# Optimization experiments

Hardware: AMD Instinct MI355X
Metric: run time of the kernel (lower is better)

## Reference

```python
import jax, jax.numpy as jnp
import numpy as np

B, T, H, L, O = 256, 512, 512, 2, 2

def setup_inputs() -> dict:
    key = jax.random.key(0)
    ks = jax.random.split(key, 9)
    s = 0.05
    return {
        "x": jax.random.normal(ks[0], (B, T), jnp.float32),
        # input-side gate weights, layer 0 (input dim 1); gate order: [r, z, n]
        "Wi0": jax.random.normal(ks[1], (3, H, 1), jnp.float32) * s,
        "bi0": jax.random.normal(ks[2], (3, H), jnp.float32) * s,
        # input-side gate weights, layers 1..L-1 (input dim H)
        "Wi_rest": jax.random.normal(ks[3], (L - 1, 3, H, H), jnp.float32) * s,
        "bi_rest": jax.random.normal(ks[4], (L - 1, 3, H), jnp.float32) * s,
        # hidden-side gate weights for all layers
        "Wh": jax.random.normal(ks[5], (L, 3, H, H), jnp.float32) * s,
        "bh": jax.random.normal(ks[6], (L, 3, H), jnp.float32) * s,
        "fc_w": jax.random.normal(ks[7], (O, H), jnp.float32) * s,
        "fc_b": jax.random.normal(ks[8], (O,), jnp.float32) * s,
    }


def reference(x, Wi0, bi0, Wi_rest, bi_rest, Wh, bh, fc_w, fc_b):
    nL = Wh.shape[0]
    hsz = Wh.shape[-1]
    bsz = x.shape[0]

    def step(h, x_t):  # h: [L, B, H], x_t: [B]
        inp = x_t[:, None]  # [B, 1]
        new_h = []
        for l in range(nL):
            # fuse the 3 input-side and 3 hidden-side gate GEMMs into one einsum each
            if l == 0:
                gi = jnp.einsum('bi,ghi->gbh', inp, Wi0) + bi0[:, None, :]
            else:
                gi = jnp.einsum('bi,ghi->gbh', inp, Wi_rest[l - 1]) + bi_rest[l - 1, :, None, :]
            gh = jnp.einsum('bi,ghi->gbh', h[l], Wh[l]) + bh[l, :, None, :]
            r = jax.nn.sigmoid(gi[0] + gh[0])
            z = jax.nn.sigmoid(gi[1] + gh[1])
            n = jnp.tanh(gi[2] + r * gh[2])
            hl = (1.0 - z) * n + z * h[l]
            new_h.append(hl)
            inp = hl
        return jnp.stack(new_h), None

    h0 = jnp.zeros((nL, bsz, hsz), x.dtype)
    h_final, _ = jax.lax.scan(step, h0, x.T)  # scan over time axis
    return h_final[-1] @ fc_w.T + fc_b  # [B, O]
```

## Files before the change

### kernel.cpp

```cpp
#include <hip/hip_runtime.h>


#define TLEN 512
#define HDIM 512
#define MROW 32
#define NL0  8
#define WPG  24
#define GRID 192
#define U0   64
#define U1   32
#define HSZ  (MROW*HDIM)
#define ROWB 1040
#define DEPTH 4

#define RT_BAR 10000000ULL

typedef __attribute__((ext_vector_type(8))) short bf16x8;
typedef __attribute__((ext_vector_type(4))) float f32x4;

#define AT_LD64(p)   __hip_atomic_load((const unsigned long long*)(p), __ATOMIC_RELAXED, __HIP_MEMORY_SCOPE_AGENT)
#define AT_LD32(p)   __hip_atomic_load((const unsigned*)(p), __ATOMIC_RELAXED, __HIP_MEMORY_SCOPE_AGENT)
#define AT_ST16(p,v) __hip_atomic_store((unsigned short*)(p), (v), __ATOMIC_RELAXED, __HIP_MEMORY_SCOPE_AGENT)
#define AT_ST32(p,v) __hip_atomic_store((unsigned*)(p), (v), __ATOMIC_RELAXED, __HIP_MEMORY_SCOPE_AGENT)
#define AT_ST32F(p,v) __hip_atomic_store((float*)(p), (v), __ATOMIC_RELAXED, __HIP_MEMORY_SCOPE_AGENT)

__device__ __forceinline__ unsigned short f2bf(float f){
  unsigned u = __builtin_bit_cast(unsigned, f);
  u = (u + 0x7FFFu + ((u>>16)&1u)) >> 16;
  return (unsigned short)u;
}
__device__ __forceinline__ float sigm(float v){ return __builtin_amdgcn_rcpf(1.f + __expf(-v)); }
__device__ __forceinline__ float tanh_f(float v){ return 1.f - 2.f*__builtin_amdgcn_rcpf(__expf(2.f*v)+1.f); }

__device__ __forceinline__ bool wait_flags(unsigned* fl, int tA, int tB, int* sab){
  if (threadIdx.x < 64){
    const int lane = threadIdx.x;
    const int tgt = (lane<8) ? tA : (lane<24 ? tB : (int)0x80000000);
    const unsigned long long t0 = __builtin_amdgcn_s_memrealtime();
    int ab = 0;
    for(;;){
      int f = (lane<24) ? (int)AT_LD32(fl + lane*16) : 0x7fffffff;
      if (__ballot(f >= tgt) == ~0ULL) break;
      if (__builtin_amdgcn_s_memrealtime() - t0 > RT_BAR){ ab = 1; break; }
      __builtin_amdgcn_s_sleep(1);
    }
    if (lane==0) *sab = ab;
  }
  __syncthreads();
  __builtin_amdgcn_sched_barrier(0);
  return *sab != 0;
}

__device__ __forceinline__ void stage16(const unsigned short* src, unsigned short* shDst, int tid){
  unsigned long long hb[16];
  #pragma unroll
  for (int i=0;i<16;++i)
    hb[i] = AT_LD64((const char*)src + tid*8 + i*2048);
  #pragma unroll
  for (int i=0;i<16;++i){
    int flat = tid*8 + i*2048;
    *(unsigned long long*)((char*)shDst + (flat>>10)*ROWB + (flat&1023)) = hb[i];
  }
}

extern "C" __global__ void __launch_bounds__(256,1)
gru_persistent(const float* __restrict__ x,
               const float* __restrict__ Wi0,
               const float* __restrict__ bi0,
               const float* __restrict__ Wi1,
               const float* __restrict__ bi1,
               const float* __restrict__ Wh,
               const float* __restrict__ bh,
               const float* __restrict__ fcw,
               const float* __restrict__ fcb,
               float* __restrict__ out,
               unsigned* __restrict__ flg,
               unsigned short* __restrict__ h0g,
               unsigned short* __restrict__ h1g,
               float* __restrict__ h1f)
{
  __shared__ unsigned short shA[MROW*(ROWB/2)];
  __shared__ unsigned short shB[MROW*(ROWB/2)];
  __shared__ float shG[MROW*192];
  __shared__ int s_ab;

  const int tid  = threadIdx.x;
  const int lane = tid & 63;
  const int w    = tid >> 6;
  const int grp  = blockIdx.x & 7;
  const int wgid = blockIdx.x >> 3;
  const int g32  = grp*32;

  unsigned* fl = flg + grp*512;
  unsigned short* h0 = h0g + grp*DEPTH*HSZ;
  unsigned short* h1 = h1g + grp*DEPTH*HSZ;

  if (wgid < NL0){
    const int u0   = wgid*U0;
    const int colb = w*48;

    bf16x8 bfr[3][16];
    #pragma unroll
    for (int nt=0; nt<3; ++nt){
      int col = colb + nt*16 + (lane&15);
      int g = col>>6, uu = col&63;
      const float* wrow = Wh + (size_t)(g*HDIM + u0 + uu)*HDIM;
      #pragma unroll
      for (int ks=0; ks<16; ++ks){
        int k = ks*32 + (lane>>4)*8;
        const float4 f0 = *(const float4*)(wrow + k);
        const float4 f1 = *(const float4*)(wrow + k + 4);
        bf16x8 v;
        v[0]=(short)f2bf(f0.x); v[1]=(short)f2bf(f0.y); v[2]=(short)f2bf(f0.z); v[3]=(short)f2bf(f0.w);
        v[4]=(short)f2bf(f1.x); v[5]=(short)f2bf(f1.y); v[6]=(short)f2bf(f1.z); v[7]=(short)f2bf(f1.w);
        bfr[nt][ks]=v;
      }
    }
    const int ua   = tid & 63;
    const int brow = (tid>>6)*8;
    float wi0v[3], bi0v[3], bh0v[3];
    #pragma unroll
    for (int g=0; g<3; ++g){
      wi0v[g] = Wi0[g*HDIM + u0+ua];
      bi0v[g] = bi0[g*HDIM + u0+ua];
      bh0v[g] = bh [g*HDIM + u0+ua];
    }
    float h_own[8];
    #pragma unroll
    for (int j=0;j<8;++j) h_own[j]=0.f;

    for (int s=0; s<TLEN; ++s){
      float xv[8];
      #pragma unroll
      for (int j=0;j<8;++j) xv[j] = x[(g32+brow+j)*TLEN + s];

      if (wait_flags(fl, s, s-3, &s_ab)) return;

      stage16(h0 + ((s-1)&3)*HSZ, shA, tid);
      __syncthreads();
      f32x4 acc[2][3] = {};
      #pragma unroll
      for (int ks=0; ks<16; ++ks){
        int koff = ks*64 + (lane>>4)*16;
        bf16x8 a0 = *(const bf16x8*)((const char*)shA + (lane&15)*ROWB + koff);
        bf16x8 a1 = *(const bf16x8*)((const char*)shA + ((lane&15)+16)*ROWB + koff);
        #pragma unroll
        for (int nt=0; nt<3; ++nt){
          acc[0][nt] = __builtin_amdgcn_mfma_f32_16x16x32_bf16(a0, bfr[nt][ks], acc[0][nt],0,0,0);
          acc[1][nt] = __builtin_amdgcn_mfma_f32_16x16x32_bf16(a1, bfr[nt][ks], acc[1][nt],0,0,0);
        }
      }
      #pragma unroll
      for (int mt=0; mt<2; ++mt)
        #pragma unroll
        for (int nt=0; nt<3; ++nt)
          #pragma unroll
          for (int j=0;j<4;++j){
            int b = mt*16 + (lane>>4)*4 + j;
            shG[b*192 + colb + nt*16 + (lane&15)] = acc[mt][nt][j];
          }
      __syncthreads();
      unsigned short* dstA = h0 + (s&3)*HSZ;
      #pragma unroll
      for (int j=0;j<8;++j){
        int b = brow + j;
        float G0 = shG[b*192 + ua]       + bh0v[0];
        float G1 = shG[b*192 + 64 + ua]  + bh0v[1];
        float G2 = shG[b*192 + 128 + ua] + bh0v[2];
        float r_ = sigm(fmaf(xv[j], wi0v[0], bi0v[0]) + G0);
        float z_ = sigm(fmaf(xv[j], wi0v[1], bi0v[1]) + G1);
        float n_ = tanh_f(fmaf(xv[j], wi0v[2], bi0v[2]) + r_*G2);
        float hn = (1.f - z_)*n_ + z_*h_own[j];
        h_own[j] = hn;
        AT_ST16(&dstA[b*HDIM + u0 + ua], f2bf(hn));
      }
      asm volatile("s_waitcnt vmcnt(0)" ::: "memory");
      __syncthreads();
      if (tid==0) AT_ST32(fl + wgid*16, (unsigned)(s+1));
    }
    if (wgid==0){
      if (wait_flags(fl, (int)0x80000000, TLEN, &s_ab)) return;
      int p = tid>>2, kl = tid&3;
      int b = p>>1, o = p&1;
      const char* h8 = (const char*)(h1f + (size_t)(g32+b)*HDIM + kl*128);
      const float2* w2 = (const float2*)(fcw + o*HDIM + kl*128);
      float a2 = 0.f;
      #pragma unroll
      for (int k=0;k<64;++k){
        unsigned long long v = AT_LD64(h8 + k*8);
        float2 hv = __builtin_bit_cast(float2, v);
        float2 wv = w2[k];
        a2 = fmaf(hv.x, wv.x, fmaf(hv.y, wv.y, a2));
      }
      a2 += __shfl_xor(a2, 1);
      a2 += __shfl_xor(a2, 2);
      if (kl==0) out[(g32+b)*2 + o] = a2 + fcb[o];
    }
  } else {
    const int u1   = (wgid-NL0)*U1;
    const int colb = (w<2) ? w*48 : 96 + (w-2)*48;

    bf16x8 bfr[3][16];
    #pragma unroll
    for (int nt=0; nt<3; ++nt){
      int col = colb + nt*16 + (lane&15);
      const float* wrow;
      if (w < 2){ int g = col>>5, uu = col&31;
        wrow = Wi1 + (size_t)(g*HDIM + u1 + uu)*HDIM;
      } else {    int c2 = col-96; int g = c2>>5, uu = c2&31;
        wrow = Wh + (size_t)((3+g)*HDIM + u1 + uu)*HDIM;
      }
      #pragma unroll
      for (int ks=0; ks<16; ++ks){
        int k = ks*32 + (lane>>4)*8;
        const float4 f0 = *(const float4*)(wrow + k);
        const float4 f1 = *(const float4*)(wrow + k + 4);
        bf16x8 v;
        v[0]=(short)f2bf(f0.x); v[1]=(short)f2bf(f0.y); v[2]=(short)f2bf(f0.z); v[3]=(short)f2bf(f0.w);
        v[4]=(short)f2bf(f1.x); v[5]=(short)f2bf(f1.y); v[6]=(short)f2bf(f1.z); v[7]=(short)f2bf(f1.w);
        bfr[nt][ks]=v;
      }
    }
    const int ua   = tid & 31;
    const int brow = (tid>>5)*4;
    float bi1v[3], bh1v[3];
    #pragma unroll
    for (int g=0; g<3; ++g){
      bi1v[g] = bi1[g*HDIM + u1+ua];
      bh1v[g] = bh [(3+g)*HDIM + u1+ua];
    }
    float h_own[4];
    #pragma unroll
    for (int j=0;j<4;++j) h_own[j]=0.f;

    for (int t=1; t<=TLEN; ++t){
      const unsigned short* srcA = h0 + ((t-1)&3)*HSZ;
      const unsigned short* srcB = h1 + ((t-2)&3)*HSZ;

      if (wait_flags(fl, (int)0x80000000, t-1, &s_ab)) return;
      unsigned long long hb1[16];
      #pragma unroll
      for (int i=0;i<16;++i)
        hb1[i] = AT_LD64((const char*)srcB + tid*8 + i*2048);

      if (wait_flags(fl, t, (int)0x80000000, &s_ab)) return;
      unsigned long long hb0[16];
      #pragma unroll
      for (int i=0;i<16;++i)
        hb0[i] = AT_LD64((const char*)srcA + tid*8 + i*2048);

      #pragma unroll
      for (int i=0;i<16;++i){
        int flat = tid*8 + i*2048;
        *(unsigned long long*)((char*)shA + (flat>>10)*ROWB + (flat&1023)) = hb0[i];
        *(unsigned long long*)((char*)shB + (flat>>10)*ROWB + (flat&1023)) = hb1[i];
      }
      __syncthreads();
      const char* shSrc = (w<2) ? (const char*)shA : (const char*)shB;
      f32x4 acc[2][3] = {};
      #pragma unroll
      for (int ks=0; ks<16; ++ks){
        int koff = ks*64 + (lane>>4)*16;
        bf16x8 a0 = *(const bf16x8*)(shSrc + (lane&15)*ROWB + koff);
        bf16x8 a1 = *(const bf16x8*)(shSrc + ((lane&15)+16)*ROWB + koff);
        #pragma unroll
        for (int nt=0; nt<3; ++nt){
          acc[0][nt] = __builtin_amdgcn_mfma_f32_16x16x32_bf16(a0, bfr[nt][ks], acc[0][nt],0,0,0);
          acc[1][nt] = __builtin_amdgcn_mfma_f32_16x16x32_bf16(a1, bfr[nt][ks], acc[1][nt],0,0,0);
        }
      }
      #pragma unroll
      for (int mt=0; mt<2; ++mt)
        #pragma unroll
        for (int nt=0; nt<3; ++nt)
          #pragma unroll
          for (int j=0;j<4;++j){
            int b = mt*16 + (lane>>4)*4 + j;
            shG[b*192 + colb + nt*16 + (lane&15)] = acc[mt][nt][j];
          }
      __syncthreads();
      unsigned short* dstB = h1 + ((t-1)&3)*HSZ;
      #pragma unroll
      for (int j=0;j<4;++j){
        int b = brow + j;
        float gi0 = shG[b*192 + ua]        + bi1v[0];
        float gi1 = shG[b*192 + 32 + ua]   + bi1v[1];
        float gi2 = shG[b*192 + 64 + ua]   + bi1v[2];
        float gh0 = shG[b*192 + 96 + ua]   + bh1v[0];
        float gh1 = shG[b*192 + 128 + ua]  + bh1v[1];
        float gh2 = shG[b*192 + 160 + ua]  + bh1v[2];
        float r_ = sigm(gi0+gh0);
        float z_ = sigm(gi1+gh1);
        float n_ = tanh_f(gi2 + r_*gh2);
        float hn = (1.f - z_)*n_ + z_*h_own[j];
        h_own[j] = hn;
        AT_ST16(&dstB[b*HDIM + u1 + ua], f2bf(hn));
        if (t == TLEN) AT_ST32F(&h1f[(size_t)(g32+b)*HDIM + u1 + ua], hn);
      }
      asm volatile("s_waitcnt vmcnt(0)" ::: "memory");
      __syncthreads();
      if (tid==0) AT_ST32(fl + wgid*16, (unsigned)t);
    }
  }
}

extern "C" void kernel_launch(void* const* d_in, const int* in_sizes, int n_in,
                              void* d_out, int out_size, void* d_ws, size_t ws_size,
                              hipStream_t stream)
{
  const float* x   = (const float*)d_in[0];
  const float* Wi0 = (const float*)d_in[1];
  const float* bi0 = (const float*)d_in[2];
  const float* Wi1 = (const float*)d_in[3];
  const float* bi1 = (const float*)d_in[4];
  const float* Wh  = (const float*)d_in[5];
  const float* bh  = (const float*)d_in[6];
  const float* fcw = (const float*)d_in[7];
  const float* fcb = (const float*)d_in[8];
  float* out = (float*)d_out;

  unsigned*       flg = (unsigned*)d_ws;
  unsigned short* h0g = (unsigned short*)((char*)d_ws + 16384);
  unsigned short* h1g = (unsigned short*)((char*)d_ws + 16384 + 1048576);
  float*          h1f = (float*)((char*)d_ws + 16384 + 2*1048576);

  hipMemsetAsync(d_ws, 0, 16384 + 2*1048576 + 524288, stream);
  gru_persistent<<<GRID, 256, 0, stream>>>(x,Wi0,bi0,Wi1,bi1,Wh,bh,fcw,fcb,out,
                                           flg,h0g,h1g,h1f);
}
```

Before: 2.420 ms.

## Split batch into 16 groups of 16 rows, doubling persistent workgroups

Halves the batch rows per group from 32 to 16 and doubles the number of independent groups, so the grid grows to 384 workgroups at two per CU. Each workgroup does half the MFMA work and half the staging loads per timestep, which shortens the serial per-step critical path. Odd groups start after a short delay to stagger their flag polling. The cost is duplicated weight registers across twice as many workgroups, two workgroups sharing each CU, and more flag-polling traffic.

```diff
diff --git a/kernel.cpp b/kernel.cpp
--- a/kernel.cpp
+++ b/kernel.cpp
@@ -3,13 +3,13 @@
 
 #define TLEN 512
 #define HDIM 512
-#define MROW 32
+#define MROW 16
 #define NL0  8
-#define WPG  24
-#define GRID 192
+#define NGRP 16
+#define GRID 384
 #define U0   64
 #define U1   32
-#define HSZ  (MROW*HDIM)
+#define HSZE (MROW*HDIM)
 #define ROWB 1040
 #define DEPTH 4
 
@@ -51,19 +51,19 @@
   return *sab != 0;
 }
 
-__device__ __forceinline__ void stage16(const unsigned short* src, unsigned short* shDst, int tid){
-  unsigned long long hb[16];
+__device__ __forceinline__ void stage8(const unsigned short* src, unsigned short* shDst, int tid){
+  unsigned long long hb[8];
   #pragma unroll
-  for (int i=0;i<16;++i)
+  for (int i=0;i<8;++i)
     hb[i] = AT_LD64((const char*)src + tid*8 + i*2048);
   #pragma unroll
-  for (int i=0;i<16;++i){
+  for (int i=0;i<8;++i){
     int flat = tid*8 + i*2048;
     *(unsigned long long*)((char*)shDst + (flat>>10)*ROWB + (flat&1023)) = hb[i];
   }
 }
 
-extern "C" __global__ void __launch_bounds__(256,1)
+extern "C" __global__ void __launch_bounds__(256,2)
 gru_persistent(const float* __restrict__ x,
                const float* __restrict__ Wi0,
                const float* __restrict__ bi0,
@@ -87,13 +87,19 @@
   const int tid  = threadIdx.x;
   const int lane = tid & 63;
   const int w    = tid >> 6;
-  const int grp  = blockIdx.x & 7;
-  const int wgid = blockIdx.x >> 3;
-  const int g32  = grp*32;
+  const int grp  = blockIdx.x & (NGRP-1);
+  const int wgid = blockIdx.x >> 4;
+  const int g16  = grp*MROW;
 
   unsigned* fl = flg + grp*512;
-  unsigned short* h0 = h0g + grp*DEPTH*HSZ;
-  unsigned short* h1 = h1g + grp*DEPTH*HSZ;
+  unsigned short* h0 = h0g + grp*DEPTH*HSZE;
+  unsigned short* h1 = h1g + grp*DEPTH*HSZE;
+
+  if (grp & 1){
+    const unsigned long long t0 = __builtin_amdgcn_s_memrealtime();
+    while (__builtin_amdgcn_s_memrealtime() - t0 < 200ULL)
+      __builtin_amdgcn_s_sleep(1);
+  }
 
   if (wgid < NL0){
     const int u0   = wgid*U0;
@@ -117,7 +123,7 @@
       }
     }
     const int ua   = tid & 63;
-    const int brow = (tid>>6)*8;
+    const int brow = (tid>>6)*4;
     float wi0v[3], bi0v[3], bh0v[3];
     #pragma unroll
     for (int g=0; g<3; ++g){
@@ -125,44 +131,39 @@
       bi0v[g] = bi0[g*HDIM + u0+ua];
       bh0v[g] = bh [g*HDIM + u0+ua];
     }
-    float h_own[8];
-    #pragma unroll
-    for (int j=0;j<8;++j) h_own[j]=0.f;
+    float h_own[4];
+    #pragma unroll
+    for (int j=0;j<4;++j) h_own[j]=0.f;
 
     for (int s=0; s<TLEN; ++s){
-      float xv[8];
-      #pragma unroll
-      for (int j=0;j<8;++j) xv[j] = x[(g32+brow+j)*TLEN + s];
+      float xv[4];
+      #pragma unroll
+      for (int j=0;j<4;++j) xv[j] = x[(g16+brow+j)*TLEN + s];
 
       if (wait_flags(fl, s, s-3, &s_ab)) return;
 
-      stage16(h0 + ((s-1)&3)*HSZ, shA, tid);
-      __syncthreads();
-      f32x4 acc[2][3] = {};
+      stage8(h0 + ((s-1)&3)*HSZE, shA, tid);
+      __syncthreads();
+      f32x4 acc[3] = {};
       #pragma unroll
       for (int ks=0; ks<16; ++ks){
         int koff = ks*64 + (lane>>4)*16;
         bf16x8 a0 = *(const bf16x8*)((const char*)shA + (lane&15)*ROWB + koff);
-        bf16x8 a1 = *(const bf16x8*)((const char*)shA + ((lane&15)+16)*ROWB + koff);
-        #pragma unroll
-        for (int nt=0; nt<3; ++nt){
-          acc[0][nt] = __builtin_amdgcn_mfma_f32_16x16x32_bf16(a0, bfr[nt][ks], acc[0][nt],0,0,0);
-          acc[1][nt] = __builtin_amdgcn_mfma_f32_16x16x32_bf16(a1, bfr[nt][ks], acc[1][nt],0,0,0);
+        #pragma unroll
+        for (int nt=0; nt<3; ++nt)
+          acc[nt] = __builtin_amdgcn_mfma_f32_16x16x32_bf16(a0, bfr[nt][ks], acc[nt],0,0,0);
+      }
+      #pragma unroll
+      for (int nt=0; nt<3; ++nt)
+        #pragma unroll
+        for (int j=0;j<4;++j){
+          int b = (lane>>4)*4 + j;
+          shG[b*192 + colb + nt*16 + (lane&15)] = acc[nt][j];
         }
-      }
-      #pragma unroll
-      for (int mt=0; mt<2; ++mt)
-        #pragma unroll
-        for (int nt=0; nt<3; ++nt)
-          #pragma unroll
-          for (int j=0;j<4;++j){
-            int b = mt*16 + (lane>>4)*4 + j;
-            shG[b*192 + colb + nt*16 + (lane&15)] = acc[mt][nt][j];
-          }
-      __syncthreads();
-      unsigned short* dstA = h0 + (s&3)*HSZ;
-      #pragma unroll
-      for (int j=0;j<8;++j){
+      __syncthreads();
+      unsigned short* dstA = h0 + (s&3)*HSZE;
+      #pragma unroll
+      for (int j=0;j<4;++j){
         int b = brow + j;
         float G0 = shG[b*192 + ua]       + bh0v[0];
         float G1 = shG[b*192 + 64 + ua]  + bh0v[1];
@@ -180,21 +181,23 @@
     }
     if (wgid==0){
       if (wait_flags(fl, (int)0x80000000, TLEN, &s_ab)) return;
-      int p = tid>>2, kl = tid&3;
-      int b = p>>1, o = p&1;
-      const char* h8 = (const char*)(h1f + (size_t)(g32+b)*HDIM + kl*128);
-      const float2* w2 = (const float2*)(fcw + o*HDIM + kl*128);
-      float a2 = 0.f;
-      #pragma unroll
-      for (int k=0;k<64;++k){
-        unsigned long long v = AT_LD64(h8 + k*8);
-        float2 hv = __builtin_bit_cast(float2, v);
-        float2 wv = w2[k];
-        a2 = fmaf(hv.x, wv.x, fmaf(hv.y, wv.y, a2));
-      }
-      a2 += __shfl_xor(a2, 1);
-      a2 += __shfl_xor(a2, 2);
-      if (kl==0) out[(g32+b)*2 + o] = a2 + fcb[o];
+      if (tid < 128){
+        int p = tid>>2, kl = tid&3;
+        int b = p>>1, o = p&1;
+        const char* h8 = (const char*)(h1f + (size_t)(g16+b)*HDIM + kl*128);
+        const float2* w2 = (const float2*)(fcw + o*HDIM + kl*128);
+        float a2 = 0.f;
+        #pragma unroll
+        for (int k=0;k<64;++k){
+          unsigned long long v = AT_LD64(h8 + k*8);
+          float2 hv = __builtin_bit_cast(float2, v);
+          float2 wv = w2[k];
+          a2 = fmaf(hv.x, wv.x, fmaf(hv.y, wv.y, a2));
+        }
+        a2 += __shfl_xor(a2, 1);
+        a2 += __shfl_xor(a2, 2);
+        if (kl==0) out[(g16+b)*2 + o] = a2 + fcb[o];
+      }
     }
   } else {
     const int u1   = (wgid-NL0)*U1;
@@ -222,66 +225,61 @@
       }
     }
     const int ua   = tid & 31;
-    const int brow = (tid>>5)*4;
+    const int brow = (tid>>5)*2;
     float bi1v[3], bh1v[3];
     #pragma unroll
     for (int g=0; g<3; ++g){
       bi1v[g] = bi1[g*HDIM + u1+ua];
       bh1v[g] = bh [(3+g)*HDIM + u1+ua];
     }
-    float h_own[4];
-    #pragma unroll
-    for (int j=0;j<4;++j) h_own[j]=0.f;
+    float h_own[2];
+    #pragma unroll
+    for (int j=0;j<2;++j) h_own[j]=0.f;
 
     for (int t=1; t<=TLEN; ++t){
-      const unsigned short* srcA = h0 + ((t-1)&3)*HSZ;
-      const unsigned short* srcB = h1 + ((t-2)&3)*HSZ;
+      const unsigned short* srcA = h0 + ((t-1)&3)*HSZE;
+      const unsigned short* srcB = h1 + ((t-2)&3)*HSZE;
 
       if (wait_flags(fl, (int)0x80000000, t-1, &s_ab)) return;
-      unsigned long long hb1[16];
-      #pragma unroll
-      for (int i=0;i<16;++i)
+      unsigned long long hb1[8];
+      #pragma unroll
+      for (int i=0;i<8;++i)
         hb1[i] = AT_LD64((const char*)srcB + tid*8 + i*2048);
 
       if (wait_flags(fl, t, (int)0x80000000, &s_ab)) return;
-      unsigned long long hb0[16];
-      #pragma unroll
-      for (int i=0;i<16;++i)
+      unsigned long long hb0[8];
+      #pragma unroll
+      for (int i=0;i<8;++i)
         hb0[i] = AT_LD64((const char*)srcA + tid*8 + i*2048);
 
       #pragma unroll
-      for (int i=0;i<16;++i){
+      for (int i=0;i<8;++i){
         int flat = tid*8 + i*2048;
         *(unsigned long long*)((char*)shA + (flat>>10)*ROWB + (flat&1023)) = hb0[i];
         *(unsigned long long*)((char*)shB + (flat>>10)*ROWB + (flat&1023)) = hb1[i];
       }
       __syncthreads();
       const char* shSrc = (w<2) ? (const char*)shA : (const char*)shB;
-      f32x4 acc[2][3] = {};
+      f32x4 acc[3] = {};
       #pragma unroll
       for (int ks=0; ks<16; ++ks){
         int koff = ks*64 + (lane>>4)*16;
         bf16x8 a0 = *(const bf16x8*)(shSrc + (lane&15)*ROWB + koff);
-        bf16x8 a1 = *(const bf16x8*)(shSrc + ((lane&15)+16)*ROWB + koff);
-        #pragma unroll
-        for (int nt=0; nt<3; ++nt){
-          acc[0][nt] = __builtin_amdgcn_mfma_f32_16x16x32_bf16(a0, bfr[nt][ks], acc[0][nt],0,0,0);
-          acc[1][nt] = __builtin_amdgcn_mfma_f32_16x16x32_bf16(a1, bfr[nt][ks], acc[1][nt],0,0,0);
+        #pragma unroll
+        for (int nt=0; nt<3; ++nt)
+          acc[nt] = __builtin_amdgcn_mfma_f32_16x16x32_bf16(a0, bfr[nt][ks], acc[nt],0,0,0);
+      }
+      #pragma unroll
+      for (int nt=0; nt<3; ++nt)
+        #pragma unroll
+        for (int j=0;j<4;++j){
+          int b = (lane>>4)*4 + j;
+          shG[b*192 + colb + nt*16 + (lane&15)] = acc[nt][j];
         }
-      }
-      #pragma unroll
-      for (int mt=0; mt<2; ++mt)
-        #pragma unroll
-        for (int nt=0; nt<3; ++nt)
-          #pragma unroll
-          for (int j=0;j<4;++j){
-            int b = mt*16 + (lane>>4)*4 + j;
-            shG[b*192 + colb + nt*16 + (lane&15)] = acc[mt][nt][j];
-          }
-      __syncthreads();
-      unsigned short* dstB = h1 + ((t-1)&3)*HSZ;
-      #pragma unroll
-      for (int j=0;j<4;++j){
+      __syncthreads();
+      unsigned short* dstB = h1 + ((t-1)&3)*HSZE;
+      #pragma unroll
+      for (int j=0;j<2;++j){
         int b = brow + j;
         float gi0 = shG[b*192 + ua]        + bi1v[0];
         float gi1 = shG[b*192 + 32 + ua]   + bi1v[1];
@@ -295,7 +293,7 @@
         float hn = (1.f - z_)*n_ + z_*h_own[j];
         h_own[j] = hn;
         AT_ST16(&dstB[b*HDIM + u1 + ua], f2bf(hn));
-        if (t == TLEN) AT_ST32F(&h1f[(size_t)(g32+b)*HDIM + u1 + ua], hn);
+        if (t == TLEN) AT_ST32F(&h1f[(size_t)(g16+b)*HDIM + u1 + ua], hn);
       }
       asm volatile("s_waitcnt vmcnt(0)" ::: "memory");
       __syncthreads();
@@ -320,11 +318,11 @@
   float* out = (float*)d_out;
 
   unsigned*       flg = (unsigned*)d_ws;
-  unsigned short* h0g = (unsigned short*)((char*)d_ws + 16384);
-  unsigned short* h1g = (unsigned short*)((char*)d_ws + 16384 + 1048576);
-  float*          h1f = (float*)((char*)d_ws + 16384 + 2*1048576);
-
-  hipMemsetAsync(d_ws, 0, 16384 + 2*1048576 + 524288, stream);
+  unsigned short* h0g = (unsigned short*)((char*)d_ws + 32768);
+  unsigned short* h1g = (unsigned short*)((char*)d_ws + 32768 + 1048576);
+  float*          h1f = (float*)((char*)d_ws + 32768 + 2*1048576);
+
+  hipMemsetAsync(d_ws, 0, 32768 + 2*1048576 + 524288, stream);
   gru_persistent<<<GRID, 256, 0, stream>>>(x,Wi0,bi0,Wi1,bi1,Wh,bh,fcw,fcb,out,
                                            flg,h0g,h1g,h1f);
 }
```

Result: faster. 2.159 ms (median of 2 runs) (-10.8%).
